# Kernel tuning notes

Hardware: AMD Instinct MI355X
Metric: run time of the kernel (lower is better)

The kernel has to match this reference:

```python
import jax, jax.numpy as jnp
import numpy as np

N_HEADS = 2
EPS = 1e-5
NEG_SLOPE = 0.02
N_CENTROIDS = 1024
RADII = (0.1, 0.2)
KS = (32, 64)


def fps(x, m):
    # Farthest point sampling (deterministic start at index 0). x: [B, C, N]
    B, C, N = x.shape
    def body(carry, _):
        distance, farthest = carry
        centroid = jnp.take_along_axis(x, jnp.broadcast_to(farthest[:, None, None], (B, C, 1)), axis=2)
        dist = jnp.sum((x - centroid) ** 2, axis=1)  # [B, N]
        distance = jnp.minimum(distance, dist)
        nxt = jnp.argmax(distance, axis=1).astype(jnp.int32)
        return (distance, nxt), farthest
    init = (jnp.full((B, N), 1e10, x.dtype), jnp.zeros((B,), jnp.int32))
    _, idxs = jax.lax.scan(body, init, None, length=m)
    return idxs.T  # [B, m]


def ball_group(x, centroids, radius, k):
    # x: [B, C, N], centroids: [B, C, M] -> (idx [B,M,k] int32, mask [B,M,k] bool)
    B, C, N = x.shape
    M = centroids.shape[2]
    d = (jnp.sum(x * x, axis=1)[:, None, :]
         - 2.0 * jnp.einsum('bcm,bcn->bmn', centroids, x)
         + jnp.sum(centroids * centroids, axis=1)[:, :, None])  # [B, M, N]
    idx = jnp.broadcast_to(jnp.arange(N, dtype=jnp.int32)[None, None, :], (B, M, N))
    idx = jnp.where(d > radius * radius, N, idx)
    idx = -jax.lax.top_k(-idx, k)[0]  # k smallest indices, ascending (matches torch.topk largest=False)
    mask = idx == N
    first = jnp.where(idx[:, :, :1] == N, 0, idx[:, :, :1])
    idx = jnp.where(mask, jnp.broadcast_to(first, idx.shape), idx)
    return idx, mask


def attention_mix(x, y, mask, wq, wk, wv, wo):
    # x: [B, C, K] centroids, y: [B, C, K, Np] groups, mask: [B, K, Np]
    B, C, K = x.shape
    Np = y.shape[3]
    H = N_HEADS
    q = jnp.einsum('oc,bck->bok', wq, x).reshape(B, H, C, K)
    kk = jnp.einsum('oc,bckn->bokn', wk, y).reshape(B, H, C, K, Np)
    v = jnp.einsum('oc,bckn->bokn', wv, y).reshape(B, H, C, K, Np)
    w = jnp.einsum('bhck,bhckn->bhkn', q, kk) / (C ** 0.5)
    w = jnp.where(mask[:, None, :, :], -1e9, w)
    w = jax.nn.softmax(w, axis=3)
    o = jnp.einsum('bhkn,bhckn->bhck', w, v).reshape(B, H * C, K)
    return jnp.einsum('oc,bck->bok', wo, o) + x


def conv_bn(x, w, b, g, beta, act):
    # 1x1 Conv1d + BatchNorm1d (training-mode batch stats) + optional LeakyReLU(0.02)
    x = jnp.einsum('oc,bck->bok', w, x) + b[None, :, None]
    mu = jnp.mean(x, axis=(0, 2), keepdims=True)
    var = jnp.var(x, axis=(0, 2), keepdims=True)
    x = (x - mu) * jax.lax.rsqrt(var + EPS) * g[None, :, None] + beta[None, :, None]
    return jnp.where(x > 0, x, NEG_SLOPE * x) if act else x


def pointnet_msg(xyz, point_features, attn_params, mlp_params):
    support = jnp.concatenate([xyz, point_features], axis=1)  # [B, 32, N]
    B, Cs, N = support.shape
    M = N_CENTROIDS
    cidx = fps(support, M)  # [B, M]
    centroids = jnp.take_along_axis(support, jnp.broadcast_to(cidx[:, None, :], (B, Cs, M)), axis=2)
    new_xyz = jnp.take_along_axis(xyz, jnp.broadcast_to(cidx[:, None, :], (B, 3, M)), axis=2)
    feats = []
    for s, (radius, k) in enumerate(zip(RADII, KS)):
        idx, mask = ball_group(support, centroids, radius, k)  # [B, M, k]
        gidx = jnp.broadcast_to(idx.reshape(B, 1, M * k), (B, Cs, M * k))
        group = jnp.take_along_axis(support, gidx, axis=2).reshape(B, Cs, M, k)
        group = group - centroids[:, :, :, None]
        f = attention_mix(centroids, group, mask, *attn_params[s])
        (w0, b0, g0, t0), (w1, b1, g1, t1) = mlp_params[s]
        f = conv_bn(f, w0, b0, g0, t0, act=True)
        f = conv_bn(f, w1, b1, g1, t1, act=False)
        feats.append(f)
    return new_xyz, jnp.concatenate(feats, axis=1)  # [B,3,M], [B,256,M]


def setup_inputs() -> dict:
    key = jax.random.key(0)
    ks = jax.random.split(key, 32)
    B, N, C = 4, 16384, 32
    d = {}
    d['xyz'] = jax.random.uniform(ks[0], (B, 3, N), jnp.float32)
    d['point_features'] = jax.random.normal(ks[1], (B, C - 3, N), jnp.float32)
    i = 2
    for s in range(2):
        d[f'aq{s}'] = 0.05 * jax.random.normal(ks[i], (64, 32), jnp.float32); i += 1
        d[f'ak{s}'] = 0.05 * jax.random.normal(ks[i], (64, 32), jnp.float32); i += 1
        d[f'av{s}'] = 0.05 * jax.random.normal(ks[i], (64, 32), jnp.float32); i += 1
        d[f'ao{s}'] = 0.05 * jax.random.normal(ks[i], (32, 64), jnp.float32); i += 1
        d[f'mw{s}0'] = 0.05 * jax.random.normal(ks[i], (64, 32), jnp.float32); i += 1
        d[f'mb{s}0'] = jnp.zeros((64,), jnp.float32)
        d[f'mg{s}0'] = jnp.ones((64,), jnp.float32)
        d[f'mbt{s}0'] = jnp.zeros((64,), jnp.float32)
        d[f'mw{s}1'] = 0.05 * jax.random.normal(ks[i], (128, 64), jnp.float32); i += 1
        d[f'mb{s}1'] = jnp.zeros((128,), jnp.float32)
        d[f'mg{s}1'] = jnp.ones((128,), jnp.float32)
        d[f'mbt{s}1'] = jnp.zeros((128,), jnp.float32)
    return d


def reference(xyz, point_features,
              aq0, ak0, av0, ao0, mw00, mb00, mg00, mbt00, mw01, mb01, mg01, mbt01,
              aq1, ak1, av1, ao1, mw10, mb10, mg10, mbt10, mw11, mb11, mg11, mbt11):
    attn_params = (((aq0, ak0, av0, ao0)), ((aq1, ak1, av1, ao1)))
    mlp_params = (((mw00, mb00, mg00, mbt00), (mw01, mb01, mg01, mbt01)),
                  ((mw10, mb10, mg10, mbt10), (mw11, mb11, mg11, mbt11)))
    return pointnet_msg(xyz, point_features, attn_params, mlp_params)
```

## Files before the change

### kernel.cpp

```cpp
#include <hip/hip_runtime.h>
#include <hip/hip_bf16.h>


static constexpr int Bb = 4;
static constexpr int Npts = 16384;
static constexpr int Mc = 1024;
static constexpr int NBLK = 16;
static constexpr int OUT_EXPECT = 12288 + 1048576;
#define BN_EPS 1e-5f
#define SLOPE 0.02f

static constexpr size_t OFF_STATS = 33024;
static constexpr size_t OFF_NORM  = 36864;
static constexpr size_t ZERO_BYTES = 65536;
static constexpr size_t OFF_CIDX  = 65536;
static constexpr size_t OFF_IDX0  = 81920;
static constexpr size_t OFF_CNT0  = 344064;
static constexpr size_t OFF_IDX1  = 360448;
static constexpr size_t OFF_CNT1  = 884736;
static constexpr size_t OFF_ATTN  = 901120;
static constexpr size_t OFF_Z0    = 1163264;
static constexpr size_t WS_REQUIRED = 1687552;
static constexpr size_t OFF_FSLOT = 901120;
static constexpr size_t FSLOT_BYTES = (size_t)Bb * Mc * NBLK * 8;

__device__ __forceinline__ float sup_at(const float* xyz, const float* pf,
                                        int b, int c, int n) {
  return (c < 3) ? xyz[((size_t)b*3 + c)*Npts + n]
                 : pf[((size_t)b*29 + (c-3))*Npts + n];
}

__device__ __forceinline__ float sanf(float v, float repl) {
  if (!(v == v) || fabsf(v) > 1e30f) v = repl;
  return v;
}

__global__ __launch_bounds__(256) void fill_kernel(float* out, int n, float val) {
  int i = blockIdx.x * 256 + threadIdx.x;
  if (i < n) out[i] = val;
}

__global__ __launch_bounds__(512, 2) void fps_kernel(
    const float* __restrict__ xyz, const float* __restrict__ pf,
    int* __restrict__ cidx, unsigned long long* __restrict__ slots) {
  const int blk = blockIdx.x;
  const int b = blk >> 4;
  const int sb = blk & (NBLK - 1);
  const int tid = threadIdx.x;
  const int lane = tid & 63, wid = tid >> 6;
  float f0[32], f1[32];
  const int p0 = sb * 1024 + tid;
  const int p1 = p0 + 512;
  float d0 = 1e10f, d1 = 1e10f;
#pragma unroll
  for (int c = 0; c < 32; ++c) {
    f0[c] = sup_at(xyz, pf, b, c, p0);
    f1[c] = sup_at(xyz, pf, b, c, p1);
  }
  __shared__ float cf[32];
  __shared__ unsigned long long red[8];
  if (sb == 0 && tid == 0) cidx[b * Mc] = 0;
  if (tid < 32) cf[tid] = sup_at(xyz, pf, b, tid, 0);
  __syncthreads();
  unsigned long long* slotb = slots + (size_t)b * Mc * NBLK;
  for (int it = 0; it < Mc - 1; ++it) {
    float cc[32];
#pragma unroll
    for (int c = 0; c < 32; ++c) cc[c] = cf[c];
    {
      float d = 0.f, e = 0.f;
#pragma unroll
      for (int c = 0; c < 32; ++c) {
        float t0 = f0[c] - cc[c];
        float s0 = __fmul_rn(t0, t0);
        d = (c == 0) ? s0 : __fadd_rn(d, s0);
        float t1 = f1[c] - cc[c];
        float s1 = __fmul_rn(t1, t1);
        e = (c == 0) ? s1 : __fadd_rn(e, s1);
      }
      d0 = fminf(d0, d);
      d1 = fminf(d1, e);
    }
    float bd; int bp;
    if (d0 >= d1) { bd = d0; bp = p0; } else { bd = d1; bp = p1; }
    unsigned long long v =
        ((unsigned long long)__float_as_uint(bd) << 32) | (unsigned int)(~(unsigned int)bp);
#pragma unroll
    for (int d = 32; d; d >>= 1) {
      unsigned long long o = __shfl_xor(v, d, 64);
      if (o > v) v = o;
    }
    if (lane == 0) red[wid] = v;
    __syncthreads();
    if (tid == 0) {
      unsigned long long vb = red[0];
#pragma unroll
      for (int w = 1; w < 8; ++w) if (red[w] > vb) vb = red[w];
      atomicMax(&slotb[(size_t)it * NBLK + sb], vb);
    }
    if (wid == 0) {
      unsigned long long myv = 0;
      if (lane < NBLK) {
        unsigned long long* sp = &slotb[(size_t)it * NBLK + lane];
        while ((myv = atomicAdd(sp, 0ull)) == 0ull) __builtin_amdgcn_s_sleep(1);
      }
      unsigned long long mv = myv;
#pragma unroll
      for (int d = 8; d; d >>= 1) {
        unsigned long long o = __shfl_xor(mv, d, 16);
        if (o > mv) mv = o;
      }
      unsigned long long vwin = __shfl(mv, 0, 64);
      int idxWin = (int)(~(unsigned int)(vwin & 0xffffffffu)) & (Npts - 1);
      if (lane < 32) cf[lane] = sup_at(xyz, pf, b, lane, idxWin);
      if (lane == 0 && sb == 0) cidx[b * Mc + it + 1] = idxWin;
    }
    __syncthreads();
  }
}

__global__ __launch_bounds__(256) void gather_kernel(
    const float* __restrict__ xyz, const int* __restrict__ cidx,
    float* __restrict__ oxyz, int out_size) {
  int idx = blockIdx.x * 256 + threadIdx.x;
  if (idx >= out_size || idx >= 12288) return;
  int m = idx & (Mc - 1);
  int t = idx >> 10;
  int b = t / 3;
  int ci = cidx[b * Mc + m] & (Npts - 1);
  oxyz[idx] = sanf(xyz[(size_t)t * Npts + ci], 888.0f);
}

__global__ __launch_bounds__(256) void ball_kernel(
    const float* __restrict__ xyz, const float* __restrict__ pf,
    const int* __restrict__ cidx,
    unsigned short* __restrict__ idx0, int* __restrict__ cnt0,
    unsigned short* __restrict__ idx1, int* __restrict__ cnt1) {
  const int b = blockIdx.x >> 6;
  const int mt = blockIdx.x & 63;
  const int tid = threadIdx.x;
  __shared__ float cf[16][32];
  __shared__ float csq[16];
  __shared__ unsigned int ent[16][128];
  __shared__ int lcnt[16];
  for (int i = tid; i < 16 * 32; i += 256) {
    int ml = i >> 5, c = i & 31;
    int ci = cidx[b * Mc + mt * 16 + ml] & (Npts - 1);
    cf[ml][c] = sup_at(xyz, pf, b, c, ci);
  }
  if (tid < 16) lcnt[tid] = 0;
  __syncthreads();
  if (tid < 16) {
    float a = 0.f;
#pragma unroll
    for (int c = 0; c < 32; ++c) a = fmaf(cf[tid][c], cf[tid][c], a);
    csq[tid] = a;
  }
  __syncthreads();
  for (int ch = 0; ch < Npts / 256; ++ch) {
    int p = ch * 256 + tid;
    float x[32];
#pragma unroll
    for (int c = 0; c < 32; ++c) x[c] = sup_at(xyz, pf, b, c, p);
    float sp = 0.f;
#pragma unroll
    for (int c = 0; c < 32; ++c) sp = fmaf(x[c], x[c], sp);
#pragma unroll 4
    for (int ml = 0; ml < 16; ++ml) {
      float dot = 0.f;
#pragma unroll
      for (int c = 0; c < 32; ++c) dot = fmaf(cf[ml][c], x[c], dot);
      float d = sp - 2.0f * dot + csq[ml];
      if (d <= 0.04f) {
        int pos = atomicAdd(&lcnt[ml], 1);
        if (pos < 128) ent[ml][pos] = (unsigned int)p | (d <= 0.01f ? 0x80000000u : 0u);
      }
    }
  }
  __syncthreads();
  if (tid < 16) {
    int ml = tid;
    int nn = lcnt[ml]; if (nn > 128) nn = 128;
    for (int i = 1; i < nn; ++i) {
      unsigned int e = ent[ml][i]; unsigned int key = e & 0x7fffffffu;
      int j = i - 1;
      while (j >= 0 && (ent[ml][j] & 0x7fffffffu) > key) { ent[ml][j+1] = ent[ml][j]; --j; }
      ent[ml][j+1] = e;
    }
    int gm = b * Mc + mt * 16 + ml;
    int c1 = nn < 64 ? nn : 64;
    unsigned short first1 = nn > 0 ? (unsigned short)(ent[ml][0] & 0x7fffffffu) : 0;
    unsigned short* o1 = idx1 + (size_t)gm * 64;
    for (int j = 0; j < 64; ++j)
      o1[j] = j < c1 ? (unsigned short)(ent[ml][j] & 0x7fffffffu) : first1;
    cnt1[gm] = c1;
    unsigned short* o0 = idx0 + (size_t)gm * 32;
    int c0 = 0; unsigned short first0 = 0;
    for (int i = 0; i < nn && c0 < 32; ++i) {
      if (ent[ml][i] & 0x80000000u) {
        unsigned short nv = (unsigned short)(ent[ml][i] & 0x7fffffffu);
        if (c0 == 0) first0 = nv;
        o0[c0++] = nv;
      }
    }
    for (int j = c0; j < 32; ++j) o0[j] = first0;
    cnt0[gm] = c0;
  }
}

template <int K>
__global__ __launch_bounds__(256) void attn_kernel(
    const float* __restrict__ xyz, const float* __restrict__ pf,
    const int* __restrict__ cidx,
    const unsigned short* __restrict__ idxS, const int* __restrict__ cntS,
    const float* __restrict__ wq, const float* __restrict__ wk,
    const float* __restrict__ wv, const float* __restrict__ wo,
    __hip_bfloat16* __restrict__ outA) {
  __shared__ float WqL[64*33], WkL[64*33], WvL[64*33], WoL[32*65];
  __shared__ float xv[4][32];
  __shared__ float qv[4][64];
  __shared__ float yb[4][2][32];
  __shared__ float ov[4][64];
  __shared__ int cns[4];
  const int tid = threadIdx.x;
  const int wid = tid >> 6, lane = tid & 63;
  const int gid = blockIdx.x;
  const int b = gid >> 8;
  const int m = ((gid & 255) << 2) + wid;
  for (int i = tid; i < 2048; i += 256) {
    int r = i >> 5, c = i & 31;
    WqL[r*33 + c] = wq[i];
    WkL[r*33 + c] = wk[i];
    WvL[r*33 + c] = wv[i];
    int ro = i >> 6, co = i & 63;
    WoL[ro*65 + co] = wo[i];
  }
  if (lane < 32) {
    int ci = cidx[b * Mc + m] & (Npts - 1);
    xv[wid][lane] = sup_at(xyz, pf, b, lane, ci);
  }
  if (lane == 0) cns[wid] = cntS[b * Mc + m];
  __syncthreads();
  {
    float acc = 0.f;
#pragma unroll
    for (int c = 0; c < 32; ++c) acc = fmaf(WqL[lane*33 + c], xv[wid][c], acc);
    qv[wid][lane] = acc;
  }
  __syncthreads();
  int cnt = cns[wid];
  cnt = cnt < 1 ? 1 : (cnt > K ? K : cnt);
  const int jj = lane < K ? lane : 0;
  int nj = (int)idxS[((size_t)b*Mc + m)*K + jj] & (Npts - 1);
  float y[32];
#pragma unroll
  for (int c = 0; c < 32; ++c)
    y[c] = sup_at(xyz, pf, b, c, nj) - xv[wid][c];
  float w0 = 0.f, w1 = 0.f;
#pragma unroll 2
  for (int r = 0; r < 32; ++r) {
    float k0 = 0.f, k1 = 0.f;
#pragma unroll
    for (int c = 0; c < 32; ++c) {
      k0 = fmaf(WkL[r*33 + c], y[c], k0);
      k1 = fmaf(WkL[(r+32)*33 + c], y[c], k1);
    }
    w0 = fmaf(qv[wid][r], k0, w0);
    w1 = fmaf(qv[wid][r+32], k1, w1);
  }
  const float iscale = 0.17677669529663689f;
  w0 *= iscale; w1 *= iscale;
  if (lane >= cnt) { w0 = -1e9f; w1 = -1e9f; }
  float mx0 = w0, mx1 = w1;
#pragma unroll
  for (int d = K/2; d; d >>= 1) {
    mx0 = fmaxf(mx0, __shfl_xor(mx0, d, K));
    mx1 = fmaxf(mx1, __shfl_xor(mx1, d, K));
  }
  float e0 = __expf(w0 - mx0), e1 = __expf(w1 - mx1);
  float s0 = e0, s1 = e1;
#pragma unroll
  for (int d = K/2; d; d >>= 1) {
    s0 += __shfl_xor(s0, d, K);
    s1 += __shfl_xor(s1, d, K);
  }
  float wn0 = e0 / s0, wn1 = e1 / s1;
#pragma unroll
  for (int c = 0; c < 32; ++c) {
    float t0 = wn0 * y[c], t1 = wn1 * y[c];
#pragma unroll
    for (int d = K/2; d; d >>= 1) {
      t0 += __shfl_xor(t0, d, K);
      t1 += __shfl_xor(t1, d, K);
    }
    if (lane == 0) { yb[wid][0][c] = t0; yb[wid][1][c] = t1; }
  }
  __syncthreads();
  {
    const int h = lane >> 5;
    float a2 = 0.f;
#pragma unroll
    for (int c = 0; c < 32; ++c) a2 = fmaf(WvL[lane*33 + c], yb[wid][h][c], a2);
    ov[wid][lane] = a2;
  }
  __syncthreads();
  if (lane < 32) {
    float a3 = 0.f;
#pragma unroll
    for (int r = 0; r < 64; ++r) a3 = fmaf(WoL[lane*65 + r], ov[wid][r], a3);
    outA[((size_t)b*32 + lane)*Mc + m] = __float2bfloat16(a3 + xv[wid][lane]);
  }
}

__global__ __launch_bounds__(256) void conv0_kernel(
    const __hip_bfloat16* __restrict__ inA, const float* __restrict__ w0,
    const float* __restrict__ b0, __hip_bfloat16* __restrict__ z0,
    float* __restrict__ ssum, float* __restrict__ ssq) {
  int idx = blockIdx.x * 256 + threadIdx.x;
  int m = idx & (Mc - 1);
  int r = (idx >> 10) & 63;
  int b = idx >> 16;
  float acc = b0[r];
#pragma unroll
  for (int c = 0; c < 32; ++c)
    acc = fmaf(w0[r*32 + c], __bfloat162float(inA[((size_t)b*32 + c)*Mc + m]), acc);
  z0[((size_t)b*64 + r)*Mc + m] = __float2bfloat16(acc);
  float s = acc, q = acc * acc;
#pragma unroll
  for (int d = 32; d; d >>= 1) { s += __shfl_down(s, d, 64); q += __shfl_down(q, d, 64); }
  if ((threadIdx.x & 63) == 0) { atomicAdd(&ssum[r], s); atomicAdd(&ssq[r], q); }
}

__global__ void bnfin_kernel(const float* __restrict__ ssum, const float* __restrict__ ssq,
    const float* __restrict__ g, const float* __restrict__ beta,
    float* __restrict__ A, float* __restrict__ Bn, int nch, float invn) {
  int r = threadIdx.x;
  if (r < nch) {
    float mu = ssum[r] * invn;
    float var = ssq[r] * invn - mu * mu;
    if (var < 0.f) var = 0.f;
    float a = g[r] * rsqrtf(var + BN_EPS);
    A[r] = a;
    Bn[r] = beta[r] - mu * a;
  }
}

template <bool WRITE>
__global__ __launch_bounds__(256) void conv1_kernel(
    const __hip_bfloat16* __restrict__ z0, const float* __restrict__ A0, const float* __restrict__ B0n,
    const float* __restrict__ w1, const float* __restrict__ b1,
    float* __restrict__ ssum, float* __restrict__ ssq,
    const float* __restrict__ A1, const float* __restrict__ B1n,
    float* __restrict__ outAll, int chOff, int out_size) {
  int idx = blockIdx.x * 256 + threadIdx.x;
  int m = idx & (Mc - 1);
  int r2 = (idx >> 10) & 127;
  int b = idx >> 17;
  float acc = b1[r2];
#pragma unroll 8
  for (int r = 0; r < 64; ++r) {
    float u = fmaf(__bfloat162float(z0[((size_t)b*64 + r)*Mc + m]), A0[r], B0n[r]);
    u = u > 0.f ? u : SLOPE * u;
    acc = fmaf(w1[r2*64 + r], u, acc);
  }
  if (WRITE) {
    float v = fmaf(acc, A1[r2], B1n[r2]);
    size_t oidx = 12288 + ((size_t)b*256 + chOff + r2)*Mc + m;
    if (oidx < (size_t)out_size) outAll[oidx] = sanf(v, 777.0f);
  } else {
    float s = acc, q = acc * acc;
#pragma unroll
    for (int d = 32; d; d >>= 1) { s += __shfl_down(s, d, 64); q += __shfl_down(q, d, 64); }
    if ((threadIdx.x & 63) == 0) { atomicAdd(&ssum[r2], s); atomicAdd(&ssq[r2], q); }
  }
}

extern "C" void kernel_launch(void* const* d_in, const int* in_sizes, int n_in,
                              void* d_out, int out_size, void* d_ws, size_t ws_size,
                              hipStream_t stream) {
  float* outb = (float*)d_out;
  int fillBlocks = (out_size + 255) / 256;
  if (n_in != 26 || in_sizes[0] != Bb*3*Npts || in_sizes[1] != Bb*29*Npts
      || in_sizes[2] != 2048) {
    fill_kernel<<<fillBlocks, 256, 0, stream>>>(outb, out_size, 7777.0f);
    return;
  }
  if (out_size != OUT_EXPECT) {
    fill_kernel<<<fillBlocks, 256, 0, stream>>>(outb, out_size, 23456.0f);
    return;
  }
  if (ws_size < WS_REQUIRED) {
    fill_kernel<<<fillBlocks, 256, 0, stream>>>(outb, out_size, 12345.0f);
    return;
  }
  const float* xyz = (const float*)d_in[0];
  const float* pf  = (const float*)d_in[1];
  char* ws = (char*)d_ws;
  int* cidx = (int*)(ws + OFF_CIDX);
  unsigned short* idx0 = (unsigned short*)(ws + OFF_IDX0);
  int* cnt0 = (int*)(ws + OFF_CNT0);
  unsigned short* idx1 = (unsigned short*)(ws + OFF_IDX1);
  int* cnt1 = (int*)(ws + OFF_CNT1);
  unsigned long long* fslots = (unsigned long long*)(ws + OFF_FSLOT);
  __hip_bfloat16* attn = (__hip_bfloat16*)(ws + OFF_ATTN);
  __hip_bfloat16* z0 = (__hip_bfloat16*)(ws + OFF_Z0);

  hipMemsetAsync(ws, 0, ZERO_BYTES, stream);
  hipMemsetAsync(ws + OFF_FSLOT, 0, FSLOT_BYTES, stream);
  fps_kernel<<<Bb*NBLK, 512, 0, stream>>>(xyz, pf, cidx, fslots);
  ball_kernel<<<Bb*64, 256, 0, stream>>>(xyz, pf, cidx, idx0, cnt0, idx1, cnt1);

  for (int s = 0; s < 2; ++s) {
    const float* aq = (const float*)d_in[2 + s*12 + 0];
    const float* ak = (const float*)d_in[2 + s*12 + 1];
    const float* av = (const float*)d_in[2 + s*12 + 2];
    const float* ao = (const float*)d_in[2 + s*12 + 3];
    const float* w0 = (const float*)d_in[2 + s*12 + 4];
    const float* b0 = (const float*)d_in[2 + s*12 + 5];
    const float* g0 = (const float*)d_in[2 + s*12 + 6];
    const float* t0 = (const float*)d_in[2 + s*12 + 7];
    const float* w1 = (const float*)d_in[2 + s*12 + 8];
    const float* b1 = (const float*)d_in[2 + s*12 + 9];
    const float* g1 = (const float*)d_in[2 + s*12 + 10];
    const float* t1 = (const float*)d_in[2 + s*12 + 11];
    float* st = (float*)(ws + OFF_STATS) + (size_t)s*384;
    float* nrm = (float*)(ws + OFF_NORM) + (size_t)s*384;
    float *sum0 = st, *sq0 = st + 64, *sum1 = st + 128, *sq1 = st + 256;
    float *A0 = nrm, *B0n = nrm + 64, *A1 = nrm + 128, *B1n = nrm + 256;
    if (s == 0)
      attn_kernel<32><<<Bb*Mc/4, 256, 0, stream>>>(xyz, pf, cidx, idx0, cnt0, aq, ak, av, ao, attn);
    else
      attn_kernel<64><<<Bb*Mc/4, 256, 0, stream>>>(xyz, pf, cidx, idx1, cnt1, aq, ak, av, ao, attn);
    conv0_kernel<<<Bb*64*Mc/256, 256, 0, stream>>>(attn, w0, b0, z0, sum0, sq0);
    bnfin_kernel<<<1, 64, 0, stream>>>(sum0, sq0, g0, t0, A0, B0n, 64, 1.0f/4096.0f);
    conv1_kernel<false><<<Bb*128*Mc/256, 256, 0, stream>>>(z0, A0, B0n, w1, b1, sum1, sq1,
                                                           nullptr, nullptr, nullptr, 0, out_size);
    bnfin_kernel<<<1, 128, 0, stream>>>(sum1, sq1, g1, t1, A1, B1n, 128, 1.0f/4096.0f);
    conv1_kernel<true><<<Bb*128*Mc/256, 256, 0, stream>>>(z0, A0, B0n, w1, b1, nullptr, nullptr,
                                                          A1, B1n, outb, s*128, out_size);
  }
  gather_kernel<<<48, 256, 0, stream>>>(xyz, cidx, outb, out_size);
}
```

Measured before the change: 2.762 ms.

## Publish winning point features through per-block mailboxes in FPS

Each FPS block's local-winner thread now writes its 32 feature values into a double-buffered mailbox in workspace before posting its slot value. After the cross-block argmax, wave 0 reads the centroid features from the winning block's mailbox instead of gathering 32 strided values from the global input arrays. The spin on slots also changes from an atomicAdd to a relaxed agent-scope atomic load. The aim is to shorten the serial per-iteration latency of the cross-block handshake. The trade is that ordering between the mailbox exchanges and the slot atomicMax rests on a fake data dependency (the DEADBEEF check) rather than a real fence, which is fragile.

After: 4.449 ms. 61.0% more time.

```diff
diff --git a/kernel.cpp b/kernel.cpp
--- a/kernel.cpp
+++ b/kernel.cpp
@@ -9,9 +9,11 @@
 static constexpr int OUT_EXPECT = 12288 + 1048576;
 #define BN_EPS 1e-5f
 #define SLOPE 0.02f
+#define SCOPE_AGT __HIP_MEMORY_SCOPE_AGENT
 
 static constexpr size_t OFF_STATS = 33024;
 static constexpr size_t OFF_NORM  = 36864;
+static constexpr size_t OFF_MBOX  = 40960;
 static constexpr size_t ZERO_BYTES = 65536;
 static constexpr size_t OFF_CIDX  = 65536;
 static constexpr size_t OFF_IDX0  = 81920;
@@ -42,7 +44,8 @@
 
 __global__ __launch_bounds__(512, 2) void fps_kernel(
     const float* __restrict__ xyz, const float* __restrict__ pf,
-    int* __restrict__ cidx, unsigned long long* __restrict__ slots) {
+    int* __restrict__ cidx, unsigned long long* __restrict__ slots,
+    unsigned long long* __restrict__ mbox) {
   const int blk = blockIdx.x;
   const int b = blk >> 4;
   const int sb = blk & (NBLK - 1);
@@ -63,7 +66,9 @@
   if (tid < 32) cf[tid] = sup_at(xyz, pf, b, tid, 0);
   __syncthreads();
   unsigned long long* slotb = slots + (size_t)b * Mc * NBLK;
+  unsigned long long* mboxb = mbox + (size_t)b * NBLK * 2 * 16;
   for (int it = 0; it < Mc - 1; ++it) {
+    const int par = it & 1;
     float cc[32];
 #pragma unroll
     for (int c = 0; c < 32; ++c) cc[c] = cf[c];
@@ -92,17 +97,39 @@
     }
     if (lane == 0) red[wid] = v;
     __syncthreads();
-    if (tid == 0) {
-      unsigned long long vb = red[0];
-#pragma unroll
-      for (int w = 1; w < 8; ++w) if (red[w] > vb) vb = red[w];
+    unsigned long long vb = red[0];
+#pragma unroll
+    for (int w = 1; w < 8; ++w) if (red[w] > vb) vb = red[w];
+    const int bpb = (int)(~(unsigned int)(vb & 0xffffffffu)) & (Npts - 1);
+    const int plocal = bpb - sb * 1024;
+    if (tid == (plocal & 511)) {
+      unsigned long long* mb = mboxb + ((size_t)sb * 2 + par) * 16;
+      unsigned long long oldOr = 0;
+      if ((plocal >> 9) == 0) {
+#pragma unroll
+        for (int c = 0; c < 16; ++c) {
+          unsigned long long pk = ((unsigned long long)__float_as_uint(f0[2*c+1]) << 32)
+                                  | __float_as_uint(f0[2*c]);
+          oldOr |= atomicExch(&mb[c], pk);
+        }
+      } else {
+#pragma unroll
+        for (int c = 0; c < 16; ++c) {
+          unsigned long long pk = ((unsigned long long)__float_as_uint(f1[2*c+1]) << 32)
+                                  | __float_as_uint(f1[2*c]);
+          oldOr |= atomicExch(&mb[c], pk);
+        }
+      }
+      if (oldOr == 0xDEADBEEFCAFEBABEull)
+        atomicAdd((unsigned int*)&slotb[(size_t)it * NBLK + sb], 0u);
       atomicMax(&slotb[(size_t)it * NBLK + sb], vb);
     }
     if (wid == 0) {
       unsigned long long myv = 0;
       if (lane < NBLK) {
-        unsigned long long* sp = &slotb[(size_t)it * NBLK + lane];
-        while ((myv = atomicAdd(sp, 0ull)) == 0ull) __builtin_amdgcn_s_sleep(1);
+        const unsigned long long* sp = &slotb[(size_t)it * NBLK + lane];
+        while ((myv = __hip_atomic_load(sp, __ATOMIC_RELAXED, SCOPE_AGT)) == 0ull)
+          __builtin_amdgcn_s_sleep(1);
       }
       unsigned long long mv = myv;
 #pragma unroll
@@ -111,9 +138,18 @@
         if (o > mv) mv = o;
       }
       unsigned long long vwin = __shfl(mv, 0, 64);
-      int idxWin = (int)(~(unsigned int)(vwin & 0xffffffffu)) & (Npts - 1);
-      if (lane < 32) cf[lane] = sup_at(xyz, pf, b, lane, idxWin);
-      if (lane == 0 && sb == 0) cidx[b * Mc + it + 1] = idxWin;
+      unsigned long long mask = __ballot(lane < NBLK && myv == vwin);
+      int sbWin = (int)__builtin_ctzll(mask);
+      if (lane < 16) {
+        unsigned long long w = __hip_atomic_load(
+            &mboxb[((size_t)sbWin * 2 + par) * 16 + lane], __ATOMIC_RELAXED, SCOPE_AGT);
+        cf[2*lane]     = __uint_as_float((unsigned int)(w & 0xffffffffu));
+        cf[2*lane + 1] = __uint_as_float((unsigned int)(w >> 32));
+      }
+      if (lane == 0 && sb == 0) {
+        int idxWin = (int)(~(unsigned int)(vwin & 0xffffffffu)) & (Npts - 1);
+        cidx[b * Mc + it + 1] = idxWin;
+      }
     }
     __syncthreads();
   }
@@ -402,12 +438,13 @@
   unsigned short* idx1 = (unsigned short*)(ws + OFF_IDX1);
   int* cnt1 = (int*)(ws + OFF_CNT1);
   unsigned long long* fslots = (unsigned long long*)(ws + OFF_FSLOT);
+  unsigned long long* mboxp = (unsigned long long*)(ws + OFF_MBOX);
   __hip_bfloat16* attn = (__hip_bfloat16*)(ws + OFF_ATTN);
   __hip_bfloat16* z0 = (__hip_bfloat16*)(ws + OFF_Z0);
 
   hipMemsetAsync(ws, 0, ZERO_BYTES, stream);
   hipMemsetAsync(ws + OFF_FSLOT, 0, FSLOT_BYTES, stream);
-  fps_kernel<<<Bb*NBLK, 512, 0, stream>>>(xyz, pf, cidx, fslots);
+  fps_kernel<<<Bb*NBLK, 512, 0, stream>>>(xyz, pf, cidx, fslots, mboxp);
   ball_kernel<<<Bb*64, 256, 0, stream>>>(xyz, pf, cidx, idx0, cnt0, idx1, cnt1);
 
   for (int s = 0; s < 2; ++s) {
```
